# Optimization experiments

Hardware: AMD Instinct MI355X
Metric: run time of the kernel (lower is better)

Reference implementation:

```python
import jax, jax.numpy as jnp
import numpy as np

V, E, H = 50000, 300, 512
T, BIO, BIO_E = 9, 10, 64
REL_E, R = 128, 50
B, L = 16, 128


def _lstm(x, wih, whh, bih, bhh):
    # x: [B, L, E]; PyTorch gate order i, f, g, o
    h0 = jnp.zeros((x.shape[0], whh.shape[1]), x.dtype)
    def step(carry, xt):
        h, c = carry
        g = xt @ wih.T + h @ whh.T + (bih + bhh)
        i, f, gg, o = jnp.split(g, 4, axis=-1)
        c = jax.nn.sigmoid(f) * c + jax.nn.sigmoid(i) * jnp.tanh(gg)
        h = jax.nn.sigmoid(o) * jnp.tanh(c)
        return (h, c), h
    _, hs = jax.lax.scan(step, (h0, h0), jnp.swapaxes(x, 0, 1))
    return jnp.swapaxes(hs, 0, 1)


def _crf_nll(emi, tags, mask, trans, start, end):
    # torchcrf-style linear-chain CRF NLL, mean reduction. emi: [B,L,T]
    mf = mask.astype(emi.dtype)
    ar = jnp.arange(emi.shape[0])
    emi_t = jnp.swapaxes(emi, 0, 1)   # [L,B,T]
    tags_t = jnp.swapaxes(tags, 0, 1)
    mf_t = jnp.swapaxes(mf, 0, 1)
    num0 = start[tags_t[0]] + emi_t[0][ar, tags_t[0]]
    def num_step(carry, inp):
        prev, score = carry
        e_t, t_t, m_t = inp
        score = score + (trans[prev, t_t] + e_t[ar, t_t]) * m_t
        prev = jnp.where(m_t > 0, t_t, prev)
        return (prev, score), None
    (last, num), _ = jax.lax.scan(num_step, (tags_t[0], num0), (emi_t[1:], tags_t[1:], mf_t[1:]))
    num = num + end[last]
    def den_step(alpha, inp):
        e_t, m_t = inp
        nxt = jax.nn.logsumexp(alpha[:, :, None] + trans[None] + e_t[:, None, :], axis=1)
        return jnp.where(m_t[:, None] > 0, nxt, alpha), None
    alpha, _ = jax.lax.scan(den_step, start[None] + emi_t[0], (emi_t[1:], mf_t[1:]))
    den = jax.nn.logsumexp(alpha + end[None], axis=1)
    return -jnp.mean(num - den)


def setup_inputs() -> dict:
    key = jax.random.key(0)
    ks = jax.random.split(key, 24)
    lengths = jax.random.randint(ks[0], (B,), L // 2, L + 1)
    tok = jax.random.randint(ks[1], (B, L), 1, V)
    tokens = jnp.where(jnp.arange(L)[None, :] < lengths[:, None], tok, 0)  # 0 = <pad>
    n = lambda k, shp, s=0.05: jax.random.normal(k, shp, dtype=jnp.float32) * s
    z = lambda shp: jnp.zeros(shp, jnp.float32)
    return dict(
        tokens=tokens,
        bio_gold=jax.random.randint(ks[2], (B, L), 0, T),
        selection_gold=jax.random.randint(ks[3], (B, L, R, L), 0, 2).astype(jnp.int32),
        is_train=1,
        word_emb=n(ks[4], (V, E), 0.02),
        rel_emb=n(ks[5], (R, REL_E), 0.1),
        bio_emb=n(ks[6], (BIO, BIO_E), 0.1),
        w_ih_f=n(ks[7], (4 * H, E)), w_hh_f=n(ks[8], (4 * H, H)),
        b_ih_f=n(ks[9], (4 * H,)), b_hh_f=n(ks[10], (4 * H,)),
        w_ih_b=n(ks[11], (4 * H, E)), w_hh_b=n(ks[12], (4 * H, H)),
        b_ih_b=n(ks[13], (4 * H,)), b_hh_b=n(ks[14], (4 * H,)),
        emission_w=n(ks[15], (T, H)), emission_b=z((T,)),
        sel_u_w=n(ks[16], (REL_E, H + BIO_E)), sel_u_b=z((REL_E,)),
        sel_v_w=n(ks[17], (REL_E, H + BIO_E)), sel_v_b=z((REL_E,)),
        sel_uv_w=n(ks[18], (REL_E, 2 * REL_E)), sel_uv_b=z((REL_E,)),
        crf_trans=n(ks[19], (T, T), 0.1),
        crf_start=n(ks[20], (T,), 0.1),
        crf_end=n(ks[21], (T,), 0.1),
    )


def reference(tokens, bio_gold, selection_gold, is_train, word_emb, rel_emb, bio_emb,
              w_ih_f, w_hh_f, b_ih_f, b_hh_f, w_ih_b, w_hh_b, b_ih_b, b_hh_b,
              emission_w, emission_b, sel_u_w, sel_u_b, sel_v_w, sel_v_b,
              sel_uv_w, sel_uv_b, crf_trans, crf_start, crf_end):
    mask = tokens != 0
    emb = word_emb[tokens]                                 # [B,L,E]
    hf = _lstm(emb, w_ih_f, w_hh_f, b_ih_f, b_hh_f)
    hb = _lstm(emb[:, ::-1], w_ih_b, w_hh_b, b_ih_b, b_hh_b)[:, ::-1]
    o = (hf + hb) * 0.5                                    # avg of the two directions
    emi = o @ emission_w.T + emission_b                    # [B,L,T]
    crf_loss = _crf_nll(emi, bio_gold, mask, crf_trans, crf_start, crf_end)
    oc = jnp.concatenate([o, bio_emb[bio_gold]], axis=-1)  # [B,L,H+BIO_E]
    u = jax.nn.relu(oc @ sel_u_w.T + sel_u_b)              # [B,L,REL_E]
    v = jax.nn.relu(oc @ sel_v_w.T + sel_v_b)
    # linear(concat(u_j, v_i)) == u_j @ W1.T + v_i @ W2.T  (fused, avoids [B,L,L,2R])
    w1, w2 = sel_uv_w[:, :REL_E], sel_uv_w[:, REL_E:]
    uv = jax.nn.relu((u @ w1.T)[:, None, :, :] + (v @ w2.T)[:, :, None, :] + sel_uv_b)  # [B,L,L,REL_E]
    logits = jnp.einsum('bijh,rh->birj', uv, rel_emb)      # [B,L,R,L]
    g = selection_gold.astype(logits.dtype)
    bce = jnp.maximum(logits, 0) - logits * g + jnp.log1p(jnp.exp(-jnp.abs(logits)))
    pm = (mask[:, :, None] & mask[:, None, :])[:, :, None, :].astype(logits.dtype)
    sel_loss = jnp.sum(bce * pm) / jnp.sum(mask).astype(logits.dtype)
    return crf_loss + sel_loss
```

## Files before the change

kernel.cpp:

```cpp
#include <hip/hip_runtime.h>
#include <math.h>

#define NB   16
#define SL   128
#define ED   300
#define HD   512
#define G4   2048
#define NT   9
#define BE   64
#define RE   128
#define NR   50
#define OCD  576
#define NTOK 2048

__device__ __forceinline__ float sigf(float x){ return 1.0f/(1.0f + __expf(-x)); }

template<int TM>
__device__ __forceinline__ void gemm_body(const float* __restrict__ A, int lda,
                                          const float* __restrict__ Bm, int ldb,
                                          float* __restrict__ C, int ldc,
                                          int N, int K,
                                          const float* __restrict__ bias1,
                                          const float* __restrict__ bias2,
                                          int do_relu, int m_blk, int n_blk)
{
    constexpr int TR = TM/16;
    __shared__ float As[16][TM+4];
    __shared__ float Bs[16][68];
    const int t = threadIdx.x;
    const int tm = (t >> 4) * TR;
    const int tn = (t & 15) * 4;
    float acc[TR][4];
    #pragma unroll
    for (int i=0;i<TR;++i){ acc[i][0]=0.f; acc[i][1]=0.f; acc[i][2]=0.f; acc[i][3]=0.f; }

    const int kc = (K + 15) >> 4;
    for (int ck = 0; ck < kc; ++ck){
        const int k0 = ck << 4;
        __syncthreads();
        #pragma unroll
        for (int it = 0; it < TM/64; ++it){
            int task = t + it*256;
            int m = task >> 2, q = task & 3;
            int kk = k0 + q*4;
            float4 v = make_float4(0.f,0.f,0.f,0.f);
            const float* ap = A + (size_t)(m_blk + m)*lda + kk;
            if (kk + 3 < K) v = *(const float4*)ap;
            else {
                if (kk   < K) v.x = ap[0];
                if (kk+1 < K) v.y = ap[1];
                if (kk+2 < K) v.z = ap[2];
            }
            As[q*4+0][m] = v.x; As[q*4+1][m] = v.y; As[q*4+2][m] = v.z; As[q*4+3][m] = v.w;
        }
        {
            int n = t >> 2, q = t & 3;
            int kk = k0 + q*4;
            int gn = n_blk + n;
            float4 v = make_float4(0.f,0.f,0.f,0.f);
            if (gn < N){
                const float* bp = Bm + (size_t)gn*ldb + kk;
                if (kk + 3 < K) v = *(const float4*)bp;
                else {
                    if (kk   < K) v.x = bp[0];
                    if (kk+1 < K) v.y = bp[1];
                    if (kk+2 < K) v.z = bp[2];
                }
            }
            Bs[q*4+0][n] = v.x; Bs[q*4+1][n] = v.y; Bs[q*4+2][n] = v.z; Bs[q*4+3][n] = v.w;
        }
        __syncthreads();
        #pragma unroll
        for (int k = 0; k < 16; ++k){
            float4 b4 = *(const float4*)&Bs[k][tn];
            float bn[4] = {b4.x, b4.y, b4.z, b4.w};
            #pragma unroll
            for (int i = 0; i < TR/4; ++i){
                float4 a4 = *(const float4*)&As[k][tm + i*4];
                float am[4] = {a4.x, a4.y, a4.z, a4.w};
                #pragma unroll
                for (int mm = 0; mm < 4; ++mm){
                    #pragma unroll
                    for (int nn = 0; nn < 4; ++nn)
                        acc[i*4+mm][nn] += am[mm]*bn[nn];
                }
            }
        }
    }
    float bv[4];
    #pragma unroll
    for (int nn=0;nn<4;++nn){
        int gn = n_blk + tn + nn;
        float bb = 0.f;
        if (gn < N){
            if (bias1) bb += bias1[gn];
            if (bias2) bb += bias2[gn];
        }
        bv[nn] = bb;
    }
    bool vec = ((ldc & 3) == 0) && (n_blk + tn + 3 < N);
    #pragma unroll
    for (int mm = 0; mm < TR; ++mm){
        int gm = m_blk + tm + mm;
        float r0 = acc[mm][0] + bv[0];
        float r1 = acc[mm][1] + bv[1];
        float r2 = acc[mm][2] + bv[2];
        float r3 = acc[mm][3] + bv[3];
        if (do_relu){ r0=fmaxf(r0,0.f); r1=fmaxf(r1,0.f); r2=fmaxf(r2,0.f); r3=fmaxf(r3,0.f); }
        if (vec){
            *(float4*)(C + (size_t)gm*ldc + n_blk + tn) = make_float4(r0,r1,r2,r3);
        } else {
            int gn = n_blk + tn;
            if (gn   < N) C[(size_t)gm*ldc + gn  ] = r0;
            if (gn+1 < N) C[(size_t)gm*ldc + gn+1] = r1;
            if (gn+2 < N) C[(size_t)gm*ldc + gn+2] = r2;
            if (gn+3 < N) C[(size_t)gm*ldc + gn+3] = r3;
        }
    }
}

template<int TM>
__global__ __launch_bounds__(256) void gemm_k(const float* __restrict__ A, int lda,
                                              const float* __restrict__ Bm, int ldb,
                                              float* __restrict__ C, int ldc,
                                              int N, int K,
                                              const float* __restrict__ bias1,
                                              const float* __restrict__ bias2,
                                              int do_relu)
{
    gemm_body<TM>(A, lda, Bm, ldb, C, ldc, N, K, bias1, bias2, do_relu,
                  blockIdx.x * TM, blockIdx.y * 64);
}

template<int TM>
__global__ __launch_bounds__(256) void gemm_dual_k(const float* __restrict__ A0, const float* __restrict__ A1, int lda,
                                                   const float* __restrict__ B0, const float* __restrict__ B1, int ldb,
                                                   float* __restrict__ C0, float* __restrict__ C1, int ldc,
                                                   int N, int K,
                                                   const float* __restrict__ bias0, const float* __restrict__ bias1,
                                                   int do_relu)
{
    const int z = blockIdx.z;
    gemm_body<TM>(z ? A1 : A0, lda, z ? B1 : B0, ldb, z ? C1 : C0, ldc, N, K,
                  z ? bias1 : bias0, nullptr, do_relu, blockIdx.x * TM, blockIdx.y * 64);
}

__global__ __launch_bounds__(256) void gemm_emb_k(const int* __restrict__ tokens,
                                                  const float* __restrict__ word_emb,
                                                  const float* __restrict__ B0, const float* __restrict__ B1,
                                                  float* __restrict__ C0, float* __restrict__ C1,
                                                  const float* __restrict__ bi0a, const float* __restrict__ bi0b,
                                                  const float* __restrict__ bi1a, const float* __restrict__ bi1b)
{
    __shared__ float As[16][132];
    __shared__ float Bs[16][68];
    const int z = blockIdx.z;
    const float* Bm = z ? B1 : B0;
    float* C       = z ? C1 : C0;
    const float* ba = z ? bi1a : bi0a;
    const float* bb = z ? bi1b : bi0b;
    const int t = threadIdx.x;
    const int m_blk = blockIdx.x * 128;
    const int n_blk = blockIdx.y * 64;
    const int tm = (t >> 4) * 8;
    const int tn = (t & 15) * 4;
    float acc[8][4];
    #pragma unroll
    for (int i=0;i<8;++i){ acc[i][0]=0.f; acc[i][1]=0.f; acc[i][2]=0.f; acc[i][3]=0.f; }

    for (int ck = 0; ck < 19; ++ck){
        const int k0 = ck << 4;
        __syncthreads();
        #pragma unroll
        for (int it = 0; it < 2; ++it){
            int task = t + it*256;
            int m = task >> 2, q = task & 3;
            int kk = k0 + q*4;
            const int tok = tokens[m_blk + m];
            const float* ap = word_emb + (size_t)tok*ED + kk;
            float4 v = make_float4(0.f,0.f,0.f,0.f);
            if (kk + 3 < ED) v = *(const float4*)ap;
            else {
                if (kk   < ED) v.x = ap[0];
                if (kk+1 < ED) v.y = ap[1];
                if (kk+2 < ED) v.z = ap[2];
            }
            As[q*4+0][m] = v.x; As[q*4+1][m] = v.y; As[q*4+2][m] = v.z; As[q*4+3][m] = v.w;
        }
        {
            int n = t >> 2, q = t & 3;
            int kk = k0 + q*4;
            const float* bp = Bm + (size_t)(n_blk + n)*ED + kk;
            float4 v = make_float4(0.f,0.f,0.f,0.f);
            if (kk + 3 < ED) v = *(const float4*)bp;
            else {
                if (kk   < ED) v.x = bp[0];
                if (kk+1 < ED) v.y = bp[1];
                if (kk+2 < ED) v.z = bp[2];
            }
            Bs[q*4+0][n] = v.x; Bs[q*4+1][n] = v.y; Bs[q*4+2][n] = v.z; Bs[q*4+3][n] = v.w;
        }
        __syncthreads();
        #pragma unroll
        for (int k = 0; k < 16; ++k){
            float4 b4 = *(const float4*)&Bs[k][tn];
            float bn[4] = {b4.x, b4.y, b4.z, b4.w};
            #pragma unroll
            for (int i = 0; i < 2; ++i){
                float4 a4 = *(const float4*)&As[k][tm + i*4];
                float am[4] = {a4.x, a4.y, a4.z, a4.w};
                #pragma unroll
                for (int mm = 0; mm < 4; ++mm){
                    #pragma unroll
                    for (int nn = 0; nn < 4; ++nn)
                        acc[i*4+mm][nn] += am[mm]*bn[nn];
                }
            }
        }
    }
    float bv[4];
    #pragma unroll
    for (int nn=0;nn<4;++nn){ int gn = n_blk + tn + nn; bv[nn] = ba[gn] + bb[gn]; }
    #pragma unroll
    for (int mm = 0; mm < 8; ++mm){
        int gm = m_blk + tm + mm;
        *(float4*)(C + (size_t)gm*G4 + n_blk + tn) =
            make_float4(acc[mm][0]+bv[0], acc[mm][1]+bv[1], acc[mm][2]+bv[2], acc[mm][3]+bv[3]);
    }
}

__device__ __forceinline__ unsigned long long agld(const unsigned long long* p){
    return __hip_atomic_load(p, __ATOMIC_RELAXED, __HIP_MEMORY_SCOPE_AGENT);
}
__device__ __forceinline__ void agst(unsigned long long* p, unsigned long long v){
    __hip_atomic_store(p, v, __ATOMIC_RELAXED, __HIP_MEMORY_SCOPE_AGENT);
}
__device__ __forceinline__ bool tagok(unsigned long long a, unsigned long long b,
                                      unsigned long long c, unsigned long long d, unsigned w){
    return ((unsigned)(a>>32)==w) & ((unsigned)(b>>32)==w) &
           ((unsigned)(c>>32)==w) & ((unsigned)(d>>32)==w);
}

__global__ __launch_bounds__(256, 2) void lstm_k(const float* __restrict__ xwf,
                                                 const float* __restrict__ xwb,
                                                 const float* __restrict__ whhf,
                                                 const float* __restrict__ whhb,
                                                 unsigned long long* __restrict__ hteam,
                                                 float* __restrict__ hf_all,
                                                 float* __restrict__ hb_all)
{
    __shared__ __align__(16) float h_s[2*HD];
    __shared__ __align__(16) float part[8*128];
    __shared__ float gates_s[128];
    __shared__ float cst[32];
    const int wg   = blockIdx.x;
    const int dir  = wg >> 8;
    const int id8  = wg & 255;
    const int team = id8 >> 5;
    const int rank = id8 & 31;
    const int b0   = team * 2;
    const int t    = threadIdx.x;
    const int wv   = t >> 6;
    const int lane = t & 63;
    const int rg   = t & 31;
    const int kc   = t >> 5;
    const int lr0  = rg*2, lr1 = rg*2 + 1;
    const int grow0 = (lr0 >> 4)*HD + rank*16 + (lr0 & 15);
    const int grow1 = (lr1 >> 4)*HD + rank*16 + (lr1 & 15);
    const float* xw   = dir ? xwb    : xwf;
    const float* whh  = dir ? whhb   : whhf;
    float*       hall = dir ? hb_all : hf_all;
    unsigned long long* hT = hteam + (size_t)((team*2 + dir)*2)*1024;

    float4 w0[16], w1[16];
    {
        const float* p0 = whh + (size_t)grow0*HD + kc*64;
        const float* p1 = whh + (size_t)grow1*HD + kc*64;
        #pragma unroll
        for (int q = 0; q < 16; ++q){
            w0[q] = *(const float4*)(p0 + q*4);
            w1[q] = *(const float4*)(p1 + q*4);
        }
    }
    const int rrow = t >> 1, rb2 = t & 1;
    const int growr = (rrow >> 4)*HD + rank*16 + (rrow & 15);
    const int ahl = t >> 1, ab2 = t & 1;
    const int hidx_a = rank*16 + ahl;
    const int s0 = wv*128 + lane;

    if (t < 32) cst[t] = 0.f;
    __syncthreads();

    int par = 0;
    for (int s = 0; s < SL; ++s){
        const unsigned want = (unsigned)s;
        const int sx = dir ? (SL-1 - s) : s;
        float xval = 0.f;
        if (t < 128)
            xval = xw[(size_t)((b0 + rb2)*SL + sx)*G4 + growr];
        {
            const unsigned long long* src = hT + (size_t)par*1024;
            unsigned long long v0, v1, v2, v3;
            for (;;){
                v0 = agld(&src[      s0     ]);
                v1 = agld(&src[      s0 + 64]);
                v2 = agld(&src[512 + s0     ]);
                v3 = agld(&src[512 + s0 + 64]);
                if (tagok(v0,v1,v2,v3,want)) break;
                __builtin_amdgcn_s_sleep(1);
            }
            h_s[     s0     ] = __uint_as_float((unsigned)v0);
            h_s[     s0 + 64] = __uint_as_float((unsigned)v1);
            h_s[HD + s0     ] = __uint_as_float((unsigned)v2);
            h_s[HD + s0 + 64] = __uint_as_float((unsigned)v3);
        }
        {
            float a00=0.f,a01=0.f,a10=0.f,a11=0.f;
            #pragma unroll
            for (int q = 0; q < 16; ++q){
                float4 wa = w0[q], wb = w1[q];
                float4 h0 = *(const float4*)(h_s + 0*HD + kc*64 + q*4);
                float4 h1 = *(const float4*)(h_s + 1*HD + kc*64 + q*4);
                a00 += wa.x*h0.x + wa.y*h0.y + wa.z*h0.z + wa.w*h0.w;
                a01 += wa.x*h1.x + wa.y*h1.y + wa.z*h1.z + wa.w*h1.w;
                a10 += wb.x*h0.x + wb.y*h0.y + wb.z*h0.z + wb.w*h0.w;
                a11 += wb.x*h1.x + wb.y*h1.y + wb.z*h1.z + wb.w*h1.w;
            }
            *(float4*)&part[kc*128 + lr0*2] = make_float4(a00,a01,a10,a11);
        }
        __syncthreads();
        if (t < 128){
            float g = 0.f;
            #pragma unroll
            for (int c = 0; c < 8; ++c) g += part[c*128 + t];
            gates_s[t] = g + xval;
        }
        __syncthreads();
        if (t < 32){
            float gi  = gates_s[(0*16 + ahl)*2 + ab2];
            float gf  = gates_s[(1*16 + ahl)*2 + ab2];
            float gc  = gates_s[(2*16 + ahl)*2 + ab2];
            float go_ = gates_s[(3*16 + ahl)*2 + ab2];
            float cp = cst[t];
            float cn = sigf(gf)*cp + sigf(gi)*tanhf(gc);
            float hn = sigf(go_)*tanhf(cn);
            cst[t] = cn;
            unsigned long long pk = ((unsigned long long)(unsigned)(s+1) << 32)
                                  | (unsigned long long)__float_as_uint(hn);
            agst(&hT[(size_t)(par^1)*1024 + ab2*512 + hidx_a], pk);
            hall[(size_t)((b0 + ab2)*SL + sx)*HD + hidx_a] = hn;
        }
        par ^= 1;
    }
}

__global__ __launch_bounds__(256) void combine_k(const float* __restrict__ hf,
                                                 const float* __restrict__ hb,
                                                 const int* __restrict__ bio_gold,
                                                 const float* __restrict__ bio_emb,
                                                 float* __restrict__ oc)
{
    int idx = blockIdx.x*256 + threadIdx.x;
    if (idx >= NTOK*144) return;
    int row = idx / 144;
    int c4 = (idx - row*144) * 4;
    float4 v;
    if (c4 < HD){
        float4 a = *(const float4*)(hf + (size_t)row*HD + c4);
        float4 b = *(const float4*)(hb + (size_t)row*HD + c4);
        v = make_float4(0.5f*(a.x+b.x), 0.5f*(a.y+b.y), 0.5f*(a.z+b.z), 0.5f*(a.w+b.w));
    } else {
        int bg = bio_gold[row];
        v = *(const float4*)(bio_emb + bg*BE + (c4 - HD));
    }
    *(float4*)(oc + (size_t)row*OCD + c4) = v;
}

__global__ __launch_bounds__(64) void crf_k(const float* __restrict__ emi,
                                            const int* __restrict__ tags,
                                            const int* __restrict__ tokens,
                                            const float* __restrict__ trans,
                                            const float* __restrict__ startv,
                                            const float* __restrict__ endv,
                                            float* __restrict__ out_crf,
                                            float* __restrict__ out_m)
{
    const int b = blockIdx.x, lane = threadIdx.x;
    unsigned long long m0 = __ballot(tokens[b*SL + lane] != 0);
    unsigned long long m1 = __ballot(tokens[b*SL + 64 + lane] != 0);
    const int len = __popcll(m0) + __popcll(m1);
    float npart = 0.f;
    #pragma unroll
    for (int half = 0; half < 2; ++half){
        int tt = lane + half*64;
        if (tt >= 1 && tt < len){
            int tp = tags[b*SL + tt - 1], tc = tags[b*SL + tt];
            npart += trans[tp*NT + tc] + emi[(size_t)(b*SL + tt)*NT + tc];
        }
    }
    #pragma unroll
    for (int off = 32; off > 0; off >>= 1) npart += __shfl_down(npart, off);
    float tr[NT]; float alpha = -1e30f;
    if (lane < NT){
        #pragma unroll
        for (int i = 0; i < NT; ++i) tr[i] = trans[i*NT + lane];
        alpha = startv[lane] + emi[(size_t)(b*SL)*NT + lane];
    }
    for (int tt = 1; tt < SL; ++tt){
        float al[NT];
        #pragma unroll
        for (int i = 0; i < NT; ++i) al[i] = __shfl(alpha, i);
        if (lane < NT && tt < len){
            float mx = -1e30f;
            #pragma unroll
            for (int i = 0; i < NT; ++i) mx = fmaxf(mx, al[i] + tr[i]);
            float se = 0.f;
            #pragma unroll
            for (int i = 0; i < NT; ++i) se += __expf(al[i] + tr[i] - mx);
            alpha = mx + __logf(se) + emi[(size_t)(b*SL + tt)*NT + lane];
        }
    }
    float alf = (lane < NT) ? (alpha + endv[lane]) : -1e30f;
    float alE[NT];
    #pragma unroll
    for (int i = 0; i < NT; ++i) alE[i] = __shfl(alf, i);
    if (lane == 0){
        float mx = -1e30f;
        #pragma unroll
        for (int i = 0; i < NT; ++i) mx = fmaxf(mx, alE[i]);
        float se = 0.f;
        #pragma unroll
        for (int i = 0; i < NT; ++i) se += __expf(alE[i] - mx);
        float den = mx + __logf(se);
        int t0g = tags[b*SL];
        float num = startv[t0g] + emi[(size_t)(b*SL)*NT + t0g] + npart;
        num += endv[tags[b*SL + len - 1]];
        atomicAdd(out_crf, -(num - den) * (1.0f/16.0f));
        atomicAdd(out_m, (float)len);
    }
}

__global__ __launch_bounds__(256) void sel_k(const float* __restrict__ U2,
                                             const float* __restrict__ V2,
                                             const float* __restrict__ uvb,
                                             const float* __restrict__ rel_emb,
                                             const int* __restrict__ gold,
                                             const int* __restrict__ tokens,
                                             float* __restrict__ out_sel)
{
    __shared__ float ret_s[RE][52];
    __shared__ float pt_s[RE][68];
    __shared__ float vb_s[RE];
    __shared__ float mk_s[64];
    __shared__ float red_s[4];
    const int jt = blockIdx.x, qi = blockIdx.y, b = blockIdx.z;
    const int t = threadIdx.x;
    if (tokens[b*SL + qi] == 0) return;
    if (t < 32){
        float4 v4 = *(const float4*)(V2 + (size_t)(b*SL + qi)*RE + t*4);
        float4 b4 = *(const float4*)(uvb + t*4);
        vb_s[t*4+0] = v4.x + b4.x; vb_s[t*4+1] = v4.y + b4.y;
        vb_s[t*4+2] = v4.z + b4.z; vb_s[t*4+3] = v4.w + b4.w;
    }
    if (t < 64) mk_s[t] = (tokens[b*SL + jt*64 + t] != 0) ? 1.f : 0.f;
    {
        int r = t & 63;
        for (int q = t >> 6; q < 32; q += 4){
            if (r < NR){
                float4 e4 = *(const float4*)(rel_emb + (size_t)r*RE + q*4);
                ret_s[q*4+0][r] = e4.x; ret_s[q*4+1][r] = e4.y;
                ret_s[q*4+2][r] = e4.z; ret_s[q*4+3][r] = e4.w;
            } else if (r < 64){
                ret_s[q*4+0][r] = 0.f; ret_s[q*4+1][r] = 0.f;
                ret_s[q*4+2][r] = 0.f; ret_s[q*4+3][r] = 0.f;
            }
        }
    }
    __syncthreads();
    {
        int j = t & 63;
        for (int q = t >> 6; q < 32; q += 4){
            float4 u4 = *(const float4*)(U2 + (size_t)(b*SL + jt*64 + j)*RE + q*4);
            pt_s[q*4+0][j] = fmaxf(u4.x + vb_s[q*4+0], 0.f);
            pt_s[q*4+1][j] = fmaxf(u4.y + vb_s[q*4+1], 0.f);
            pt_s[q*4+2][j] = fmaxf(u4.z + vb_s[q*4+2], 0.f);
            pt_s[q*4+3][j] = fmaxf(u4.w + vb_s[q*4+3], 0.f);
        }
    }
    __syncthreads();
    const int mj = (t & 15) * 4;
    const int nr = (t >> 4) * 4;
    float accv[4][4];
    #pragma unroll
    for (int i=0;i<4;++i){ accv[i][0]=0.f; accv[i][1]=0.f; accv[i][2]=0.f; accv[i][3]=0.f; }
    #pragma unroll 4
    for (int k = 0; k < RE; ++k){
        float4 aj = *(const float4*)&pt_s[k][mj];
        float4 br = *(const float4*)&ret_s[k][nr];
        float am[4] = {aj.x, aj.y, aj.z, aj.w};
        float bn[4] = {br.x, br.y, br.z, br.w};
        #pragma unroll
        for (int mm = 0; mm < 4; ++mm){
            #pragma unroll
            for (int nn = 0; nn < 4; ++nn)
                accv[mm][nn] += am[mm]*bn[nn];
        }
    }
    float lsum = 0.f;
    #pragma unroll
    for (int nn = 0; nn < 4; ++nn){
        int r = nr + nn;
        if (r < NR){
            const int* gp = gold + (size_t)((b*SL + qi)*NR + r)*SL + jt*64 + mj;
            #pragma unroll
            for (int mm = 0; mm < 4; ++mm){
                float l = accv[mm][nn];
                float g = (float)gp[mm];
                float bce = fmaxf(l, 0.f) - l*g + __logf(1.f + __expf(-fabsf(l)));
                lsum += bce * mk_s[mj + mm];
            }
        }
    }
    #pragma unroll
    for (int off = 32; off > 0; off >>= 1) lsum += __shfl_down(lsum, off);
    if ((t & 63) == 0) red_s[t >> 6] = lsum;
    __syncthreads();
    if (t == 0) atomicAdd(out_sel, red_s[0]+red_s[1]+red_s[2]+red_s[3]);
}

__global__ void finalize_k(const float* __restrict__ accum, float* __restrict__ out)
{
    if (threadIdx.x == 0 && blockIdx.x == 0) out[0] = accum[0] + accum[1] / accum[2];
}

extern "C" void kernel_launch(void* const* d_in, const int* in_sizes, int n_in,
                              void* d_out, int out_size, void* d_ws, size_t ws_size,
                              hipStream_t stream)
{
    const int*   tokens    = (const int*)  d_in[0];
    const int*   bio_gold  = (const int*)  d_in[1];
    const int*   sel_gold  = (const int*)  d_in[2];
    const float* word_emb  = (const float*)d_in[4];
    const float* rel_emb   = (const float*)d_in[5];
    const float* bio_emb   = (const float*)d_in[6];
    const float* w_ih_f    = (const float*)d_in[7];
    const float* w_hh_f    = (const float*)d_in[8];
    const float* b_ih_f    = (const float*)d_in[9];
    const float* b_hh_f    = (const float*)d_in[10];
    const float* w_ih_b    = (const float*)d_in[11];
    const float* w_hh_b    = (const float*)d_in[12];
    const float* b_ih_b    = (const float*)d_in[13];
    const float* b_hh_b    = (const float*)d_in[14];
    const float* emission_w= (const float*)d_in[15];
    const float* emission_b= (const float*)d_in[16];
    const float* sel_u_w   = (const float*)d_in[17];
    const float* sel_u_b   = (const float*)d_in[18];
    const float* sel_v_w   = (const float*)d_in[19];
    const float* sel_v_b   = (const float*)d_in[20];
    const float* sel_uv_w  = (const float*)d_in[21];
    const float* sel_uv_b  = (const float*)d_in[22];
    const float* crf_trans = (const float*)d_in[23];
    const float* crf_start = (const float*)d_in[24];
    const float* crf_end   = (const float*)d_in[25];
    (void)in_sizes; (void)n_in; (void)out_size; (void)ws_size;

    float* ws     = (float*)d_ws;
    float* emb    = ws;
    float* xwf    = emb    + (size_t)NTOK*ED;
    float* xwb    = xwf    + (size_t)NTOK*G4;
    float* hf_all = xwb    + (size_t)NTOK*G4;
    float* hb_all = hf_all + (size_t)NTOK*HD;
    float* oc     = hb_all + (size_t)NTOK*HD;
    float* emi    = oc     + (size_t)NTOK*OCD;
    float* u_     = emi    + (size_t)NTOK*NT;
    float* v_     = u_     + (size_t)NTOK*RE;
    float* U2     = v_     + (size_t)NTOK*RE;
    float* V2     = U2     + (size_t)NTOK*RE;
    float* accum  = V2     + (size_t)NTOK*RE;

    unsigned long long* hteam = (unsigned long long*)emb;

    hipMemsetAsync(accum, 0, 4*sizeof(float), stream);
    hipMemsetAsync(hteam, 0, (size_t)8*2*2*1024*sizeof(unsigned long long), stream);

    gemm_emb_k<<<dim3(NTOK/128, G4/64, 2), 256, 0, stream>>>(tokens, word_emb,
                                                             w_ih_f, w_ih_b, xwf, xwb,
                                                             b_ih_f, b_hh_f, b_ih_b, b_hh_b);

    {
        const float *p_xwf = xwf, *p_xwb = xwb, *p_whf = w_hh_f, *p_whb = w_hh_b;
        unsigned long long* p_ht = hteam;
        float *p_hf = hf_all, *p_hb = hb_all;
        void* args[7] = {&p_xwf, &p_xwb, &p_whf, &p_whb, &p_ht, &p_hf, &p_hb};
        hipLaunchCooperativeKernel(lstm_k, dim3(512), dim3(256), args, 0u, stream);
    }

    combine_k<<<(NTOK*144 + 255)/256, 256, 0, stream>>>(hf_all, hb_all, bio_gold, bio_emb, oc);

    gemm_k<64><<<dim3(NTOK/64, 1), 256, 0, stream>>>(oc, OCD, emission_w, HD, emi, NT, NT, HD, emission_b, nullptr, 0);
    gemm_dual_k<64><<<dim3(NTOK/64, 2, 2), 256, 0, stream>>>(oc, oc, OCD, sel_u_w, sel_v_w, OCD,
                                                             u_, v_, RE, RE, OCD, sel_u_b, sel_v_b, 1);
    gemm_dual_k<64><<<dim3(NTOK/64, 2, 2), 256, 0, stream>>>(u_, v_, RE, sel_uv_w, sel_uv_w + RE, 2*RE,
                                                             U2, V2, RE, RE, RE, nullptr, nullptr, 0);

    crf_k<<<NB, 64, 0, stream>>>(emi, bio_gold, tokens, crf_trans, crf_start, crf_end, accum + 0, accum + 2);
    sel_k<<<dim3(2, SL, NB), 256, 0, stream>>>(U2, V2, sel_uv_b, rel_emb, sel_gold, tokens, accum + 1);

    finalize_k<<<1, 1, 0, stream>>>(accum, (float*)d_out);
}
```

Before: 865.3 us.

## Split LSTM hidden-state exchange into plain data plus per-rank ready flags

Each LSTM step used to publish the new hidden state as 64-bit values that paired every float with its step tag, and readers polled all 2048 tagged words until every tag matched. Now the hidden values are stored as plain 32-bit floats. Each workgroup publishes one step flag per rank after a vmcnt wait, and readers spin on only 32 flags before loading the data once as packed 64-bit pairs. This is meant to cut the polling traffic and the size of the data exchanged on the serial critical path. The cost is an extra wait and flag store per step, and correctness now depends on store ordering and visibility, which relaxed atomics without an explicit acquire/release fence only partly guarantee.

```diff
diff --git a/kernel.cpp b/kernel.cpp
--- a/kernel.cpp
+++ b/kernel.cpp
@@ -229,23 +229,22 @@
     }
 }
 
-__device__ __forceinline__ unsigned long long agld(const unsigned long long* p){
+__device__ __forceinline__ unsigned long long agld64(const unsigned long long* p){
     return __hip_atomic_load(p, __ATOMIC_RELAXED, __HIP_MEMORY_SCOPE_AGENT);
 }
-__device__ __forceinline__ void agst(unsigned long long* p, unsigned long long v){
+__device__ __forceinline__ unsigned agld32(const unsigned* p){
+    return __hip_atomic_load(p, __ATOMIC_RELAXED, __HIP_MEMORY_SCOPE_AGENT);
+}
+__device__ __forceinline__ void agst32(unsigned* p, unsigned v){
     __hip_atomic_store(p, v, __ATOMIC_RELAXED, __HIP_MEMORY_SCOPE_AGENT);
-}
-__device__ __forceinline__ bool tagok(unsigned long long a, unsigned long long b,
-                                      unsigned long long c, unsigned long long d, unsigned w){
-    return ((unsigned)(a>>32)==w) & ((unsigned)(b>>32)==w) &
-           ((unsigned)(c>>32)==w) & ((unsigned)(d>>32)==w);
 }
 
 __global__ __launch_bounds__(256, 2) void lstm_k(const float* __restrict__ xwf,
                                                  const float* __restrict__ xwb,
                                                  const float* __restrict__ whhf,
                                                  const float* __restrict__ whhb,
-                                                 unsigned long long* __restrict__ hteam,
+                                                 float* __restrict__ hdat,
+                                                 unsigned* __restrict__ tags,
                                                  float* __restrict__ hf_all,
                                                  float* __restrict__ hb_all)
 {
@@ -260,7 +259,6 @@
     const int rank = id8 & 31;
     const int b0   = team * 2;
     const int t    = threadIdx.x;
-    const int wv   = t >> 6;
     const int lane = t & 63;
     const int rg   = t & 31;
     const int kc   = t >> 5;
@@ -270,7 +268,8 @@
     const float* xw   = dir ? xwb    : xwf;
     const float* whh  = dir ? whhb   : whhf;
     float*       hall = dir ? hb_all : hf_all;
-    unsigned long long* hT = hteam + (size_t)((team*2 + dir)*2)*1024;
+    float*    hD  = hdat + (size_t)((team*2 + dir)*2)*1024;
+    unsigned* tgp = tags + (size_t)((team*2 + dir)*2)*32;
 
     float4 w0[16], w1[16];
     {
@@ -286,7 +285,6 @@
     const int growr = (rrow >> 4)*HD + rank*16 + (rrow & 15);
     const int ahl = t >> 1, ab2 = t & 1;
     const int hidx_a = rank*16 + ahl;
-    const int s0 = wv*128 + lane;
 
     if (t < 32) cst[t] = 0.f;
     __syncthreads();
@@ -299,20 +297,20 @@
         if (t < 128)
             xval = xw[(size_t)((b0 + rb2)*SL + sx)*G4 + growr];
         {
-            const unsigned long long* src = hT + (size_t)par*1024;
-            unsigned long long v0, v1, v2, v3;
-            for (;;){
-                v0 = agld(&src[      s0     ]);
-                v1 = agld(&src[      s0 + 64]);
-                v2 = agld(&src[512 + s0     ]);
-                v3 = agld(&src[512 + s0 + 64]);
-                if (tagok(v0,v1,v2,v3,want)) break;
-                __builtin_amdgcn_s_sleep(1);
-            }
-            h_s[     s0     ] = __uint_as_float((unsigned)v0);
-            h_s[     s0 + 64] = __uint_as_float((unsigned)v1);
-            h_s[HD + s0     ] = __uint_as_float((unsigned)v2);
-            h_s[HD + s0 + 64] = __uint_as_float((unsigned)v3);
+            const unsigned* tp = tgp + par*32;
+            if (lane < 32){
+                while (agld32(&tp[lane]) != want)
+                    __builtin_amdgcn_s_sleep(1);
+            }
+        }
+        {
+            const unsigned long long* ds = (const unsigned long long*)(hD + par*1024);
+            unsigned long long a = agld64(&ds[t]);
+            unsigned long long b = agld64(&ds[t + 256]);
+            *(float2*)&h_s[2*t] =
+                make_float2(__uint_as_float((unsigned)a), __uint_as_float((unsigned)(a>>32)));
+            *(float2*)&h_s[HD + 2*t] =
+                make_float2(__uint_as_float((unsigned)b), __uint_as_float((unsigned)(b>>32)));
         }
         {
             float a00=0.f,a01=0.f,a10=0.f,a11=0.f;
@@ -345,9 +343,11 @@
             float cn = sigf(gf)*cp + sigf(gi)*tanhf(gc);
             float hn = sigf(go_)*tanhf(cn);
             cst[t] = cn;
-            unsigned long long pk = ((unsigned long long)(unsigned)(s+1) << 32)
-                                  | (unsigned long long)__float_as_uint(hn);
-            agst(&hT[(size_t)(par^1)*1024 + ab2*512 + hidx_a], pk);
+            agst32((unsigned*)&hD[(size_t)(par^1)*1024 + ab2*512 + hidx_a],
+                   __float_as_uint(hn));
+            asm volatile("s_waitcnt vmcnt(0)" ::: "memory");
+            if (t == 0)
+                agst32(&tgp[(par^1)*32 + rank], (unsigned)(s + 1));
             hall[(size_t)((b0 + ab2)*SL + sx)*HD + hidx_a] = hn;
         }
         par ^= 1;
@@ -578,10 +578,11 @@
     float* V2     = U2     + (size_t)NTOK*RE;
     float* accum  = V2     + (size_t)NTOK*RE;
 
-    unsigned long long* hteam = (unsigned long long*)emb;
+    float*    hdat  = emb;
+    unsigned* htags = (unsigned*)(hdat + 8*2*2*1024);
 
     hipMemsetAsync(accum, 0, 4*sizeof(float), stream);
-    hipMemsetAsync(hteam, 0, (size_t)8*2*2*1024*sizeof(unsigned long long), stream);
+    hipMemsetAsync(hdat, 0, (size_t)(8*2*2*1024*4 + 8*2*2*32*4), stream);
 
     gemm_emb_k<<<dim3(NTOK/128, G4/64, 2), 256, 0, stream>>>(tokens, word_emb,
                                                              w_ih_f, w_ih_b, xwf, xwb,
@@ -589,9 +590,10 @@
 
     {
         const float *p_xwf = xwf, *p_xwb = xwb, *p_whf = w_hh_f, *p_whb = w_hh_b;
-        unsigned long long* p_ht = hteam;
+        float* p_hd = hdat;
+        unsigned* p_tg = htags;
         float *p_hf = hf_all, *p_hb = hb_all;
-        void* args[7] = {&p_xwf, &p_xwb, &p_whf, &p_whb, &p_ht, &p_hf, &p_hb};
+        void* args[8] = {&p_xwf, &p_xwb, &p_whf, &p_whb, &p_hd, &p_tg, &p_hf, &p_hb};
         hipLaunchCooperativeKernel(lstm_k, dim3(512), dim3(256), args, 0u, stream);
     }
 
```

Measured after the change: 1.160 ms. 1.34x slower.
